# Kernel optimization log

Hardware: AMD Instinct MI355X
Metric: run time of the kernel (lower is better)

The kernel has to match this reference:

```python
import jax, jax.numpy as jnp
import numpy as np

B, N, M, J, D, PF = 4, 131072, 10475, 55, 64, 486


def setup_inputs() -> dict:
    key = jax.random.key(0)
    ks = jax.random.split(key, 16)
    return {
        "pts": jax.random.normal(ks[0], (B, N, 3), jnp.float32),
        "betas": jax.random.normal(ks[1], (B, 10), jnp.float32),
        "pose_feature": jax.random.normal(ks[2], (B, PF), jnp.float32),
        "init_spdir": jax.random.normal(ks[3], (M, 3, 10), jnp.float32),
        "init_podir": jax.random.normal(ks[4], (PF, 3 * M), jnp.float32),
        "init_faces": jax.random.randint(ks[5], (N, 3), 0, M, jnp.int32),
        "tfs_A": jax.random.normal(ks[6], (B, J, 4, 4), jnp.float32),
        "tfs_inv": jax.random.normal(ks[7], (1, J, 4, 4), jnp.float32),
        "poseoff_cano": jax.random.normal(ks[8], (1, N, 3), jnp.float32),
        "lbsw": jax.random.uniform(ks[9], (1, N, J), jnp.float32),
        "lbs_voxel": jax.random.uniform(ks[10], (1, J, D, D, D), jnp.float32),
        "vox_scale": jnp.ones((1, 1, 3), jnp.float32),
        "vox_offset": jnp.zeros((1, 1, 3), jnp.float32),
        "mask": jax.random.randint(ks[11], (B, N), 0, 2, jnp.int32),
    }


def _trilinear(vox, x, scale, offset):
    # vox: [J,D,D,D], x: [b,n,3] -> [b,n,J] trilinearly interpolated weights
    nj, nd = vox.shape[0], vox.shape[-1]
    g = jnp.clip(x * scale + offset, -1.0, 1.0)          # normalized coords
    t = (g + 1.0) * 0.5 * (nd - 1)                        # voxel coords
    i0 = jnp.clip(jnp.floor(t), 0, nd - 2).astype(jnp.int32)
    f = t - i0                                            # fractional part
    vf = vox.reshape(nj, -1)                              # [J, D^3]
    out = jnp.zeros(x.shape[:-1] + (nj,), x.dtype)
    for dx in (0, 1):
        for dy in (0, 1):
            for dz in (0, 1):
                ix = i0[..., 0] + dx
                iy = i0[..., 1] + dy
                iz = i0[..., 2] + dz
                wgt = ((f[..., 0] if dx else 1.0 - f[..., 0]) *
                       (f[..., 1] if dy else 1.0 - f[..., 1]) *
                       (f[..., 2] if dz else 1.0 - f[..., 2]))
                fid = (ix * nd + iy) * nd + iz            # flat voxel index [b,n]
                out = out + wgt[..., None] * jnp.moveaxis(vf[:, fid], 0, -1)
    return out


def reference(pts, betas, pose_feature, init_spdir, init_podir, init_faces,
              tfs_A, tfs_inv, poseoff_cano, lbsw, lbs_voxel, vox_scale,
              vox_offset, mask):
    b, n, _ = pts.shape
    # blend-shape offsets on template vertices
    shape_full = jnp.einsum('bl,mkl->bmk', betas, init_spdir)      # [b,M,3]
    pose_full = (pose_feature @ init_podir).reshape(b, -1, 3)      # [b,M,3]
    # face-vertex gather then average over the 3 vertices of each face
    shape_off = shape_full[:, init_faces].mean(axis=2)             # [b,F,3]
    pose_off = pose_full[:, init_faces].mean(axis=2)               # [b,F,3]
    x = pts + shape_off + pose_off - poseoff_cano                  # canonical pts + offsets
    # voxel-grid skinning-weight lookup at canonical points
    w_vox = _trilinear(lbs_voxel[0], pts, vox_scale, vox_offset)   # [b,n,J]
    w = jnp.where(mask[..., None] > 0, lbsw, w_vox)
    w = w / jnp.clip(w.sum(-1, keepdims=True), 1e-8)
    # per-point blended transforms: A @ A_inv_template
    tfs = tfs_A @ tfs_inv                                          # [b,J,4,4]
    T = jnp.einsum('bnj,bjrc->bnrc', w, tfs)                       # [b,n,4,4]
    xh = jnp.concatenate([x, jnp.ones_like(x[..., :1])], axis=-1)
    posed = jnp.einsum('bnrc,bnc->bnr', T, xh)[..., :3]
    return posed.reshape(b, n, 1, 3), T
```

## Files before the change

kernel.cpp:

```cpp
#include <hip/hip_runtime.h>

#define B_  4
#define N_  131072
#define J_  55
#define JP_ 56
#define D_  64
#define D3_ 262144
#define PF_ 486
#define COLS_ 31425

#define GZ_ 2048
#define OZ_ 123

#define BL16(u) __uint_as_float((u) << 16)
#define BH16(u) __uint_as_float((u) & 0xffff0000u)

typedef float f4a __attribute__((ext_vector_type(4), aligned(4)));

__device__ __forceinline__ unsigned short f2bf(float v) {
    unsigned u = __float_as_uint(v);
    u += 0x7fffu + ((u >> 16) & 1u);
    return (unsigned short)(u >> 16);
}

__device__ __forceinline__ void stage_tfs(int b, int tid,
                                          const float* __restrict__ A,
                                          const float* __restrict__ Ainv,
                                          float* __restrict__ dst) {
#pragma unroll
    for (int base = 0; base < 896; base += 256) {
        int idx = base + tid;
        if (idx < 896) {
            int j = idx >> 4, rc = idx & 15, r = rc >> 2, c = rc & 3;
            float v = 0.f;
            if (j < J_) {
#pragma unroll
                for (int k = 0; k < 4; ++k)
                    v += A[((b * J_ + j) * 4 + r) * 4 + k] *
                         Ainv[(j * 4 + k) * 4 + c];
            }
            dst[idx] = v;
        }
    }
}

#define GACC(gv, q)                                         \
    {   float4 t0 = s4[(q) * 4 + 0], t1 = s4[(q) * 4 + 1],  \
               t2 = s4[(q) * 4 + 2], t3 = s4[(q) * 4 + 3];  \
        gv[0]  += w * t0.x; gv[1]  += w * t0.y;             \
        gv[2]  += w * t0.z; gv[3]  += w * t0.w;             \
        gv[4]  += w * t1.x; gv[5]  += w * t1.y;             \
        gv[6]  += w * t1.z; gv[7]  += w * t1.w;             \
        gv[8]  += w * t2.x; gv[9]  += w * t2.y;             \
        gv[10] += w * t2.z; gv[11] += w * t2.w;             \
        gv[12] += w * t3.x; gv[13] += w * t3.y;             \
        gv[14] += w * t3.z; gv[15] += w * t3.w; }

__global__ __launch_bounds__(256) void k_prelude(
    const float* __restrict__ A, const float* __restrict__ Ainv,
    const float* __restrict__ vox,
    uint4* __restrict__ Gtb, float* __restrict__ Stb,
    const float* __restrict__ pf, const float* __restrict__ podir,
    const float* __restrict__ betas, const float* __restrict__ spdir,
    float* __restrict__ off_full) {
    int bx = blockIdx.x;
    int tid = threadIdx.x;

    if (bx < GZ_) {
        __shared__ float stfs[2 * 896];
        int bp = (bx & 4) >> 2;
        int chunk = ((bx >> 3) << 2) | (bx & 3);
        stage_tfs(2 * bp + 0, tid, A, Ainv, stfs);
        stage_tfs(2 * bp + 1, tid, A, Ainv, stfs + 896);
        __syncthreads();

        int v = chunk * 256 + tid;
        float g0[16], g1[16];
#pragma unroll
        for (int r = 0; r < 16; ++r) { g0[r] = 0.f; g1[r] = 0.f; }
        float s = 0.f;
        const float4* sa = (const float4*)stfs;
        const float4* sb = (const float4*)(stfs + 896);
        float wa[11], wb[11];
#pragma unroll
        for (int k = 0; k < 11; ++k) wa[k] = vox[(size_t)k * D3_ + v];
        for (int j0 = 0; j0 < J_; j0 += 11) {
            if (j0 + 11 < J_) {
#pragma unroll
                for (int k = 0; k < 11; ++k)
                    wb[k] = vox[(size_t)(j0 + 11 + k) * D3_ + v];
            }
#pragma unroll
            for (int k = 0; k < 11; ++k) {
                float w = wa[k];
                s += w;
                int j = j0 + k;
                { const float4* s4 = sa; GACC(g0, j) }
                { const float4* s4 = sb; GACC(g1, j) }
            }
#pragma unroll
            for (int k = 0; k < 11; ++k) wa[k] = wb[k];
        }
        if (bp == 0) Stb[v] = s;
#pragma unroll
        for (int bb = 0; bb < 2; ++bb) {
            float* g = bb ? g1 : g0;
            unsigned gw[8];
#pragma unroll
            for (int k = 0; k < 8; ++k)
                gw[k] = (unsigned)f2bf(g[2 * k]) |
                        ((unsigned)f2bf(g[2 * k + 1]) << 16);
            uint4* gp = Gtb + ((size_t)(2 * bp + bb) * D3_ + v) * 2;
            gp[0] = make_uint4(gw[0], gw[1], gw[2], gw[3]);
            gp[1] = make_uint4(gw[4], gw[5], gw[6], gw[7]);
        }
    } else {
        int col = (bx - GZ_) * 256 + tid;
        if (col >= COLS_) return;
        float a0 = 0.f, a1 = 0.f, a2 = 0.f, a3 = 0.f;
        {
            float sp[10];
#pragma unroll
            for (int l = 0; l < 10; ++l) sp[l] = spdir[col * 10 + l];
#pragma unroll
            for (int l = 0; l < 10; ++l) {
                a0 += betas[0 * 10 + l] * sp[l];
                a1 += betas[1 * 10 + l] * sp[l];
                a2 += betas[2 * 10 + l] * sp[l];
                a3 += betas[3 * 10 + l] * sp[l];
            }
        }
        int p = 0;
        for (; p + 16 <= PF_; p += 16) {
            float v16[16];
#pragma unroll
            for (int k = 0; k < 16; ++k)
                v16[k] = podir[(size_t)(p + k) * COLS_ + col];
#pragma unroll
            for (int k = 0; k < 16; ++k) {
                a0 += pf[0 * PF_ + p + k] * v16[k];
                a1 += pf[1 * PF_ + p + k] * v16[k];
                a2 += pf[2 * PF_ + p + k] * v16[k];
                a3 += pf[3 * PF_ + p + k] * v16[k];
            }
        }
        for (; p < PF_; ++p) {
            float v = podir[(size_t)p * COLS_ + col];
            a0 += pf[0 * PF_ + p] * v;
            a1 += pf[1 * PF_ + p] * v;
            a2 += pf[2 * PF_ + p] * v;
            a3 += pf[3 * PF_ + p] * v;
        }
        off_full[0 * COLS_ + col] = a0;
        off_full[1 * COLS_ + col] = a1;
        off_full[2 * COLS_ + col] = a2;
        off_full[3 * COLS_ + col] = a3;
    }
}

#define ACC8(Toff, qa, qb)                                 \
    T[Toff + 0] += w0 * BL16(qa.x) + w1 * BL16(qb.x);      \
    T[Toff + 1] += w0 * BH16(qa.x) + w1 * BH16(qb.x);      \
    T[Toff + 2] += w0 * BL16(qa.y) + w1 * BL16(qb.y);      \
    T[Toff + 3] += w0 * BH16(qa.y) + w1 * BH16(qb.y);      \
    T[Toff + 4] += w0 * BL16(qa.z) + w1 * BL16(qb.z);      \
    T[Toff + 5] += w0 * BH16(qa.z) + w1 * BH16(qb.z);      \
    T[Toff + 6] += w0 * BL16(qa.w) + w1 * BL16(qb.w);      \
    T[Toff + 7] += w0 * BH16(qa.w) + w1 * BH16(qb.w);

__global__ __launch_bounds__(256) void k_main(
    const float* __restrict__ pts, const int* __restrict__ faces,
    const float* __restrict__ poseoff, const int* __restrict__ mask,
    const float* __restrict__ vox_scale, const float* __restrict__ vox_offset,
    const float* __restrict__ off_full,
    const float* __restrict__ A, const float* __restrict__ Ainv,
    const float* __restrict__ lbsw, const uint4* __restrict__ Gtb,
    const float* __restrict__ Stb,
    float* __restrict__ out_posed, float* __restrict__ out_T) {
    __shared__ float sx0[256], sx1[256], sx2[256];
    __shared__ float sf0[256], sf1[256], sf2[256];
    __shared__ int   scell[256];
    __shared__ unsigned short lst[256];
    __shared__ int wc[4];
    __shared__ float stfs[896];

    int bid = blockIdx.x;
    int b  = (bid & 7) >> 1;
    int nc = ((bid >> 3) << 1) | (bid & 1);
    int tid = threadIdx.x;
    int n = nc * 256 + tid;
    int i = (b << 17) | n;

    stage_tfs(b, tid, A, Ainv, stfs);

    float px = pts[3 * i + 0], py = pts[3 * i + 1], pz = pts[3 * i + 2];
    int f0 = faces[3 * n + 0], f1 = faces[3 * n + 1], f2 = faces[3 * n + 2];
    const float* ob = off_full + b * COLS_;
    const float c3 = 1.f / 3.f;
    float ox = (ob[f0 * 3 + 0] + ob[f1 * 3 + 0] + ob[f2 * 3 + 0]) * c3;
    float oy = (ob[f0 * 3 + 1] + ob[f1 * 3 + 1] + ob[f2 * 3 + 1]) * c3;
    float oz = (ob[f0 * 3 + 2] + ob[f1 * 3 + 2] + ob[f2 * 3 + 2]) * c3;
    sx0[tid] = px + ox - poseoff[3 * n + 0];
    sx1[tid] = py + oy - poseoff[3 * n + 1];
    sx2[tid] = pz + oz - poseoff[3 * n + 2];

    bool isv = !(mask[i] > 0);
    if (isv) {
        float sxc = vox_scale[0], syc = vox_scale[1], szc = vox_scale[2];
        float o0 = vox_offset[0], o1 = vox_offset[1], o2 = vox_offset[2];
        float gx = fminf(fmaxf(px * sxc + o0, -1.f), 1.f);
        float gy = fminf(fmaxf(py * syc + o1, -1.f), 1.f);
        float gz = fminf(fmaxf(pz * szc + o2, -1.f), 1.f);
        float tx = (gx + 1.f) * 0.5f * (D_ - 1);
        float ty = (gy + 1.f) * 0.5f * (D_ - 1);
        float tz = (gz + 1.f) * 0.5f * (D_ - 1);
        int ix = (int)floorf(tx); if (ix > D_ - 2) ix = D_ - 2; if (ix < 0) ix = 0;
        int iy = (int)floorf(ty); if (iy > D_ - 2) iy = D_ - 2; if (iy < 0) iy = 0;
        int iz = (int)floorf(tz); if (iz > D_ - 2) iz = D_ - 2; if (iz < 0) iz = 0;
        sf0[tid] = tx - ix;
        sf1[tid] = ty - iy;
        sf2[tid] = tz - iz;
        scell[tid] = (ix * D_ + iy) * D_ + iz;
    }

    unsigned long long bal = __ballot(isv);
    int lane = tid & 63, wid = tid >> 6;
    if (lane == 0) wc[wid] = __popcll(bal);
    __syncthreads();
    int pre = 0;
#pragma unroll
    for (int k = 0; k < 4; ++k) pre += (k < wid) ? wc[k] : 0;
    int tot = wc[0] + wc[1] + wc[2] + wc[3];
    unsigned long long lt = ((unsigned long long)1 << lane) - 1ull;
    int vbefore = pre + __popcll(bal & lt);
    int pos = isv ? vbefore : (tot + (tid - vbefore));
    lst[pos] = (unsigned short)tid;
    __syncthreads();

    int slot = lst[tid];
    float x0 = sx0[slot], x1 = sx1[slot], x2 = sx2[slot];
    int ii = (b << 17) | (nc * 256 + slot);

    float T[16];
#pragma unroll
    for (int r = 0; r < 16; ++r) T[r] = 0.f;
    float wsum = 0.f;

    if (tid < tot) {
        float fx = sf0[slot], fy = sf1[slot], fz = sf2[slot];
        int cell = scell[slot];
        const uint4* Gb = Gtb + (size_t)b * D3_ * 2;
#pragma unroll
        for (int cc = 0; cc < 4; ++cc) {
            int fid = cell + ((cc & 2) ? D_ * D_ : 0) + ((cc & 1) ? D_ : 0);
            float wxy = ((cc & 2) ? fx : 1.f - fx) * ((cc & 1) ? fy : 1.f - fy);
            float w0 = wxy * (1.f - fz);
            float w1 = wxy * fz;
            const uint4* R = Gb + (size_t)fid * 2;
            uint4 q0 = R[0], q1 = R[1], q2 = R[2], q3 = R[3];
            wsum += w0 * Stb[fid] + w1 * Stb[fid + 1];
            ACC8(0, q0, q2)
            ACC8(8, q1, q3)
        }
    } else {
        int n2 = nc * 256 + slot;
        const float* lw = lbsw + (size_t)n2 * J_;
        f4a q[13];
#pragma unroll
        for (int k = 0; k < 13; ++k)
            q[k] = *(const f4a*)(lw + 4 * k);
        float w52 = lw[52], w53 = lw[53], w54 = lw[54];
        const float4* s4 = (const float4*)stfs;
#pragma unroll
        for (int k = 0; k < 13; ++k) {
#pragma unroll
            for (int m = 0; m < 4; ++m) {
                float w = q[k][m];
                wsum += w;
                GACC(T, k * 4 + m)
            }
        }
        float wt[3] = { w52, w53, w54 };
#pragma unroll
        for (int m = 0; m < 3; ++m) {
            float w = wt[m];
            wsum += w;
            GACC(T, 52 + m)
        }
    }

    float inv = 1.f / fmaxf(wsum, 1e-8f);
    float t[16];
#pragma unroll
    for (int r = 0; r < 16; ++r) t[r] = T[r] * inv;
    out_posed[3 * ii + 0] = t[0] * x0 + t[1] * x1 + t[2] * x2 + t[3];
    out_posed[3 * ii + 1] = t[4] * x0 + t[5] * x1 + t[6] * x2 + t[7];
    out_posed[3 * ii + 2] = t[8] * x0 + t[9] * x1 + t[10] * x2 + t[11];
    float4* to = (float4*)(out_T + (size_t)ii * 16);
    to[0] = make_float4(t[0], t[1], t[2], t[3]);
    to[1] = make_float4(t[4], t[5], t[6], t[7]);
    to[2] = make_float4(t[8], t[9], t[10], t[11]);
    to[3] = make_float4(t[12], t[13], t[14], t[15]);
}

extern "C" void kernel_launch(void* const* d_in, const int* in_sizes, int n_in,
                              void* d_out, int out_size, void* d_ws, size_t ws_size,
                              hipStream_t stream) {
    const float* pts      = (const float*)d_in[0];
    const float* betas    = (const float*)d_in[1];
    const float* pf       = (const float*)d_in[2];
    const float* spdir    = (const float*)d_in[3];
    const float* podir    = (const float*)d_in[4];
    const int*   faces    = (const int*)d_in[5];
    const float* tfs_A    = (const float*)d_in[6];
    const float* tfs_inv  = (const float*)d_in[7];
    const float* poseoff  = (const float*)d_in[8];
    const float* lbsw     = (const float*)d_in[9];
    const float* vox      = (const float*)d_in[10];
    const float* vscale   = (const float*)d_in[11];
    const float* voffset  = (const float*)d_in[12];
    const int*   mask     = (const int*)d_in[13];

    char* w = (char*)d_ws;
    uint4* Gtb      = (uint4*)w;
    float* Stb      = (float*)(w + 33554432);
    float* off_full = (float*)(w + 34603008);

    float* out_posed = (float*)d_out;
    float* out_T     = out_posed + (size_t)B_ * N_ * 3;

    k_prelude<<<GZ_ + OZ_, 256, 0, stream>>>(
        tfs_A, tfs_inv, vox, Gtb, Stb, pf, podir, betas, spdir, off_full);
    k_main<<<2048, 256, 0, stream>>>(pts, faces, poseoff, mask, vscale,
                                     voffset, off_full, tfs_A, tfs_inv,
                                     lbsw, Gtb, Stb, out_posed, out_T);
}
```

Before: 307.7 us.

## Store joint transforms as bf16 in LDS and regroup prelude by batch

The per-joint blended transforms staged in shared memory are now packed as bf16 pairs, which halves LDS footprint and read traffic in both kernels. The prelude is also reorganised so each block handles one batch and two voxels per thread instead of two batches per voxel. Each unpacked transform row is then reused for both voxels, while the voxel weights are loaded once per batch rather than once per batch pair. The cost is reduced precision in the transform coefficients, extra unpack ALU work, and roughly twice the global voxel reads overall.

```diff
diff --git a/kernel.cpp b/kernel.cpp
--- a/kernel.cpp
+++ b/kernel.cpp
@@ -23,38 +23,39 @@
     return (unsigned short)(u >> 16);
 }
 
-__device__ __forceinline__ void stage_tfs(int b, int tid,
-                                          const float* __restrict__ A,
-                                          const float* __restrict__ Ainv,
-                                          float* __restrict__ dst) {
-#pragma unroll
-    for (int base = 0; base < 896; base += 256) {
+__device__ __forceinline__ void stage_tfs_bf16(int b, int tid,
+                                               const float* __restrict__ A,
+                                               const float* __restrict__ Ainv,
+                                               unsigned* __restrict__ dst) {
+#pragma unroll
+    for (int base = 0; base < 448; base += 256) {
         int idx = base + tid;
-        if (idx < 896) {
-            int j = idx >> 4, rc = idx & 15, r = rc >> 2, c = rc & 3;
-            float v = 0.f;
+        if (idx < 448) {
+            int j = idx >> 3, pp = idx & 7;
+            float e0 = 0.f, e1 = 0.f;
             if (j < J_) {
-#pragma unroll
-                for (int k = 0; k < 4; ++k)
-                    v += A[((b * J_ + j) * 4 + r) * 4 + k] *
-                         Ainv[(j * 4 + k) * 4 + c];
-            }
-            dst[idx] = v;
+                int r = pp >> 1, c0 = (pp & 1) * 2;
+#pragma unroll
+                for (int k = 0; k < 4; ++k) {
+                    float av = A[((b * J_ + j) * 4 + r) * 4 + k];
+                    e0 += av * Ainv[(j * 4 + k) * 4 + c0];
+                    e1 += av * Ainv[(j * 4 + k) * 4 + c0 + 1];
+                }
+            }
+            dst[idx] = (unsigned)f2bf(e0) | ((unsigned)f2bf(e1) << 16);
         }
     }
 }
 
-#define GACC(gv, q)                                         \
-    {   float4 t0 = s4[(q) * 4 + 0], t1 = s4[(q) * 4 + 1],  \
-               t2 = s4[(q) * 4 + 2], t3 = s4[(q) * 4 + 3];  \
-        gv[0]  += w * t0.x; gv[1]  += w * t0.y;             \
-        gv[2]  += w * t0.z; gv[3]  += w * t0.w;             \
-        gv[4]  += w * t1.x; gv[5]  += w * t1.y;             \
-        gv[6]  += w * t1.z; gv[7]  += w * t1.w;             \
-        gv[8]  += w * t2.x; gv[9]  += w * t2.y;             \
-        gv[10] += w * t2.z; gv[11] += w * t2.w;             \
-        gv[12] += w * t3.x; gv[13] += w * t3.y;             \
-        gv[14] += w * t3.z; gv[15] += w * t3.w; }
+#define UNP16(t, q0, q1)                                        \
+    t[0]  = BL16(q0.x); t[1]  = BH16(q0.x);                     \
+    t[2]  = BL16(q0.y); t[3]  = BH16(q0.y);                     \
+    t[4]  = BL16(q0.z); t[5]  = BH16(q0.z);                     \
+    t[6]  = BL16(q0.w); t[7]  = BH16(q0.w);                     \
+    t[8]  = BL16(q1.x); t[9]  = BH16(q1.x);                     \
+    t[10] = BL16(q1.y); t[11] = BH16(q1.y);                     \
+    t[12] = BL16(q1.z); t[13] = BH16(q1.z);                     \
+    t[14] = BL16(q1.w); t[15] = BH16(q1.w);
 
 __global__ __launch_bounds__(256) void k_prelude(
     const float* __restrict__ A, const float* __restrict__ Ainv,
@@ -67,50 +68,62 @@
     int tid = threadIdx.x;
 
     if (bx < GZ_) {
-        __shared__ float stfs[2 * 896];
-        int bp = (bx & 4) >> 2;
-        int chunk = ((bx >> 3) << 2) | (bx & 3);
-        stage_tfs(2 * bp + 0, tid, A, Ainv, stfs);
-        stage_tfs(2 * bp + 1, tid, A, Ainv, stfs + 896);
+        __shared__ unsigned stfsb[448];
+        int b = (bx & 7) >> 1;
+        int chunk = ((bx >> 3) << 1) | (bx & 1);
+        stage_tfs_bf16(b, tid, A, Ainv, stfsb);
         __syncthreads();
 
-        int v = chunk * 256 + tid;
+        int v0 = chunk * 512 + tid;
         float g0[16], g1[16];
 #pragma unroll
         for (int r = 0; r < 16; ++r) { g0[r] = 0.f; g1[r] = 0.f; }
-        float s = 0.f;
-        const float4* sa = (const float4*)stfs;
-        const float4* sb = (const float4*)(stfs + 896);
-        float wa[11], wb[11];
-#pragma unroll
-        for (int k = 0; k < 11; ++k) wa[k] = vox[(size_t)k * D3_ + v];
-        for (int j0 = 0; j0 < J_; j0 += 11) {
-            if (j0 + 11 < J_) {
-#pragma unroll
-                for (int k = 0; k < 11; ++k)
-                    wb[k] = vox[(size_t)(j0 + 11 + k) * D3_ + v];
-            }
-#pragma unroll
-            for (int k = 0; k < 11; ++k) {
-                float w = wa[k];
-                s += w;
+        float s0 = 0.f, s1 = 0.f;
+        const uint4* s16 = (const uint4*)stfsb;
+        float wa[5][2], wb[5][2];
+#pragma unroll
+        for (int k = 0; k < 5; ++k) {
+            wa[k][0] = vox[(size_t)k * D3_ + v0];
+            wa[k][1] = vox[(size_t)k * D3_ + v0 + 256];
+        }
+        for (int j0 = 0; j0 < J_; j0 += 5) {
+            if (j0 + 5 < J_) {
+#pragma unroll
+                for (int k = 0; k < 5; ++k) {
+                    wb[k][0] = vox[(size_t)(j0 + 5 + k) * D3_ + v0];
+                    wb[k][1] = vox[(size_t)(j0 + 5 + k) * D3_ + v0 + 256];
+                }
+            }
+#pragma unroll
+            for (int k = 0; k < 5; ++k) {
                 int j = j0 + k;
-                { const float4* s4 = sa; GACC(g0, j) }
-                { const float4* s4 = sb; GACC(g1, j) }
-            }
-#pragma unroll
-            for (int k = 0; k < 11; ++k) wa[k] = wb[k];
-        }
-        if (bp == 0) Stb[v] = s;
-#pragma unroll
-        for (int bb = 0; bb < 2; ++bb) {
-            float* g = bb ? g1 : g0;
+                uint4 q0 = s16[j * 2], q1 = s16[j * 2 + 1];
+                float t[16];
+                UNP16(t, q0, q1)
+                float w0 = wa[k][0], w1 = wa[k][1];
+                s0 += w0; s1 += w1;
+#pragma unroll
+                for (int r = 0; r < 16; ++r) {
+                    g0[r] += w0 * t[r];
+                    g1[r] += w1 * t[r];
+                }
+            }
+#pragma unroll
+            for (int k = 0; k < 5; ++k) {
+                wa[k][0] = wb[k][0]; wa[k][1] = wb[k][1];
+            }
+        }
+        if (b == 0) { Stb[v0] = s0; Stb[v0 + 256] = s1; }
+#pragma unroll
+        for (int m = 0; m < 2; ++m) {
+            float* g = m ? g1 : g0;
+            int v = v0 + m * 256;
             unsigned gw[8];
 #pragma unroll
             for (int k = 0; k < 8; ++k)
                 gw[k] = (unsigned)f2bf(g[2 * k]) |
                         ((unsigned)f2bf(g[2 * k + 1]) << 16);
-            uint4* gp = Gtb + ((size_t)(2 * bp + bb) * D3_ + v) * 2;
+            uint4* gp = Gtb + ((size_t)b * D3_ + v) * 2;
             gp[0] = make_uint4(gw[0], gw[1], gw[2], gw[3]);
             gp[1] = make_uint4(gw[4], gw[5], gw[6], gw[7]);
         }
@@ -182,7 +195,7 @@
     __shared__ int   scell[256];
     __shared__ unsigned short lst[256];
     __shared__ int wc[4];
-    __shared__ float stfs[896];
+    __shared__ unsigned stfsb[448];
 
     int bid = blockIdx.x;
     int b  = (bid & 7) >> 1;
@@ -191,7 +204,7 @@
     int n = nc * 256 + tid;
     int i = (b << 17) | n;
 
-    stage_tfs(b, tid, A, Ainv, stfs);
+    stage_tfs_bf16(b, tid, A, Ainv, stfsb);
 
     float px = pts[3 * i + 0], py = pts[3 * i + 1], pz = pts[3 * i + 2];
     int f0 = faces[3 * n + 0], f1 = faces[3 * n + 1], f2 = faces[3 * n + 2];
@@ -269,23 +282,18 @@
 #pragma unroll
         for (int k = 0; k < 13; ++k)
             q[k] = *(const f4a*)(lw + 4 * k);
-        float w52 = lw[52], w53 = lw[53], w54 = lw[54];
-        const float4* s4 = (const float4*)stfs;
-#pragma unroll
-        for (int k = 0; k < 13; ++k) {
-#pragma unroll
-            for (int m = 0; m < 4; ++m) {
-                float w = q[k][m];
-                wsum += w;
-                GACC(T, k * 4 + m)
-            }
-        }
-        float wt[3] = { w52, w53, w54 };
-#pragma unroll
-        for (int m = 0; m < 3; ++m) {
-            float w = wt[m];
+        float wt0 = lw[52], wt1 = lw[53], wt2 = lw[54];
+        const uint4* s16 = (const uint4*)stfsb;
+#pragma unroll
+        for (int jj = 0; jj < J_; ++jj) {
+            float w = (jj < 52) ? q[jj >> 2][jj & 3]
+                                : (jj == 52 ? wt0 : (jj == 53 ? wt1 : wt2));
             wsum += w;
-            GACC(T, 52 + m)
+            uint4 a0 = s16[jj * 2], a1 = s16[jj * 2 + 1];
+            float t[16];
+            UNP16(t, a0, a1)
+#pragma unroll
+            for (int r = 0; r < 16; ++r) T[r] += w * t[r];
         }
     }
 
```

Result: no change. 303.8 us (-1.3%).
